# Kernel tuning notes

Measured on AMD Instinct MI355X. Metric: run time of the kernel, lower is better.

The kernel has to match this reference:

```python
import jax, jax.numpy as jnp
import numpy as np

D_MODEL = 1024
N_HEADS = 16
D_K = D_MODEL // N_HEADS
ROPE_BASE = 10000.0


def _rope_cos_sin(seq_len, dim):
    # matches calc_rope_theta: freqs over even indices of head dim
    freqs = jnp.arange(0, dim, 2, dtype=jnp.float32) / dim
    inv_freq = 1.0 / (ROPE_BASE ** freqs)                      # [dim/2]
    pos = jnp.arange(seq_len, dtype=jnp.float32)               # [S]
    ang = pos[:, None] * inv_freq[None, :]                     # [S, dim/2]
    return jnp.cos(ang), jnp.sin(ang)


def _apply_rope(x, cos, sin):
    # x: [N, S, dk]; complex pairs are consecutive elements (view_as_complex)
    x0 = x[..., 0::2]
    x1 = x[..., 1::2]
    r = x0 * cos - x1 * sin
    i = x0 * sin + x1 * cos
    return jnp.stack([r, i], axis=-1).reshape(x.shape)


def setup_inputs() -> dict:
    key = jax.random.key(0)
    ks = jax.random.split(key, 11)
    B, S, D = 4, 1024, D_MODEL
    w = lambda k: jax.random.normal(k, (D, D), dtype=jnp.float32) * 0.02
    b = lambda k: jax.random.normal(k, (D,), dtype=jnp.float32) * 0.02
    return {
        "q": jax.random.normal(ks[0], (B, S, D), dtype=jnp.float32),
        "k": jax.random.normal(ks[1], (B, S, D), dtype=jnp.float32),
        "v": jax.random.normal(ks[2], (B, S, D), dtype=jnp.float32),
        "Wq": w(ks[3]), "bq": b(ks[4]),
        "Wk": w(ks[5]), "bk": b(ks[6]),
        "Wv": w(ks[7]), "bv": b(ks[8]),
        "Wo": w(ks[9]), "bo": b(ks[10]),
    }


def reference(q, k, v, Wq, bq, Wk, bk, Wv, bv, Wo, bo):
    B, S, D = q.shape
    H, dk = N_HEADS, D_K
    qp = (q @ Wq + bq).reshape(B, S, H, dk)
    kp = (k @ Wk + bk).reshape(B, S, H, dk)
    vp = (v @ Wv + bv).reshape(B, S, H, dk)

    cos, sin = _rope_cos_sin(S, dk)
    # Faithful to source: raw reshape (B,S,H,dk)->(-1,S,dk) before RoPE
    qp = _apply_rope(qp.reshape(-1, S, dk), cos, sin).reshape(B, S, H, dk)
    kp = _apply_rope(kp.reshape(-1, S, dk), cos, sin).reshape(B, S, H, dk)

    qh = qp.transpose(0, 2, 1, 3)  # [B,H,S,dk]
    kh = kp.transpose(0, 2, 1, 3)
    vh = vp.transpose(0, 2, 1, 3)

    scores = jnp.einsum("bhqd,bhkd->bhqk", qh, kh) / jnp.sqrt(jnp.float32(dk))
    attn = jax.nn.softmax(scores, axis=-1)
    out = jnp.einsum("bhqk,bhkd->bhqd", attn, vh)
    out = out.transpose(0, 2, 1, 3).reshape(B, S, D)
    return out @ Wo + bo
```

## Files before the change

### kernel.cpp

```cpp
#include <hip/hip_runtime.h>

typedef __attribute__((ext_vector_type(8))) short bf16x8;
typedef __attribute__((ext_vector_type(4))) short short4v;
typedef __attribute__((ext_vector_type(4))) float f32x4;

#define MFMA16x16x32(a, b, c) __builtin_amdgcn_mfma_f32_16x16x32_bf16((a), (b), (c), 0, 0, 0)

__device__ __forceinline__ short f2bf(float f) {
    unsigned u = __builtin_bit_cast(unsigned, f);
    u += 0x7FFFu + ((u >> 16) & 1u);
    return (short)(u >> 16);
}

__device__ __forceinline__ void gl_lds16(const void* g, void* l) {
    __builtin_amdgcn_global_load_lds((__attribute__((address_space(1))) void*)g,
                                     (__attribute__((address_space(3))) void*)l,
                                     16, 0, 0);
}

__device__ __forceinline__ void cvt16(const float* __restrict__ p, bf16x8& lo, bf16x8& hi) {
    f32x4 a = *(const f32x4*)(p);
    f32x4 b = *(const f32x4*)(p + 4);
    f32x4 c = *(const f32x4*)(p + 8);
    f32x4 d = *(const f32x4*)(p + 12);
#pragma unroll
    for (int i = 0; i < 4; ++i) {
        lo[i]     = f2bf(a[i]);
        lo[i + 4] = f2bf(b[i]);
        hi[i]     = f2bf(c[i]);
        hi[i + 4] = f2bf(d[i]);
    }
}

__global__ __launch_bounds__(256) void cvt3(const float* __restrict__ x0,
                                            const float* __restrict__ x1,
                                            const float* __restrict__ x2,
                                            short* __restrict__ y) {
    int sel = blockIdx.y;
    const float* x = sel == 0 ? x0 : (sel == 1 ? x1 : x2);
    short* yy = y + (size_t)sel * (1 << 22);
    int i = (blockIdx.x * 256 + threadIdx.x) * 16;
    bf16x8 lo, hi;
    cvt16(x + i, lo, hi);
    *(bf16x8*)(yy + i)     = lo;
    *(bf16x8*)(yy + i + 8) = hi;
}

__global__ __launch_bounds__(256) void transW4(const float* __restrict__ w0,
                                               const float* __restrict__ w1,
                                               const float* __restrict__ w2,
                                               const float* __restrict__ w3,
                                               short* __restrict__ wt) {
    __shared__ short t[64][80];
    int z = blockIdx.z;
    const float* W = z == 0 ? w0 : (z == 1 ? w1 : (z == 2 ? w2 : w3));
    short* Wt = wt + (size_t)z * (1 << 20);
    int bx = blockIdx.x, by = blockIdx.y;
    int tid = threadIdx.x;
    int sr = tid >> 2, sc = (tid & 3) * 16;
    bf16x8 lo, hi;
    cvt16(W + (by * 64 + sr) * 1024 + bx * 64 + sc, lo, hi);
    *(bf16x8*)&t[sr][sc]     = lo;
    *(bf16x8*)&t[sr][sc + 8] = hi;
    __syncthreads();
    bf16x8 o0, o1;
#pragma unroll
    for (int i = 0; i < 8; ++i) {
        o0[i] = t[sc + i][sr];
        o1[i] = t[sc + 8 + i][sr];
    }
    short* dst = Wt + (bx * 64 + sr) * 1024 + by * 64 + sc;
    *(bf16x8*)(dst)     = o0;
    *(bf16x8*)(dst + 8) = o1;
}

template <int MODE>
__global__ __launch_bounds__(256) void gemm_nt(const short* __restrict__ A,
                                               const short* __restrict__ Bt,
                                               const float* __restrict__ bias,
                                               void* __restrict__ dstv) {
    __shared__ short As[128 * 64];
    __shared__ short Bs[64 * 64];
    const int K = 1024;
    int tid = threadIdx.x;
    int bn = blockIdx.x, bm = blockIdx.y;
    int wave = tid >> 6, lane = tid & 63;
    int quad = lane >> 4, l16 = lane & 15;
    int wm = (wave >> 1) * 64, wn = (wave & 1) * 32;

    f32x4 acc[4][2] = {};

    for (int kb = 0; kb < K; kb += 64) {
#pragma unroll
        for (int j = 0; j < 4; ++j) {
            int c = j * 256 + tid;
            gl_lds16(A + (bm * 128 + (c >> 3)) * K + kb + (c & 7) * 8, As + c * 8);
        }
#pragma unroll
        for (int j = 0; j < 2; ++j) {
            int c = j * 256 + tid;
            gl_lds16(Bt + (bn * 64 + (c >> 3)) * K + kb + (c & 7) * 8, Bs + c * 8);
        }
        __syncthreads();
#pragma unroll
        for (int ks = 0; ks < 2; ++ks) {
            bf16x8 bf0 = *(const bf16x8*)&Bs[(wn + l16) * 64 + ks * 32 + quad * 8];
            bf16x8 bf1 = *(const bf16x8*)&Bs[(wn + 16 + l16) * 64 + ks * 32 + quad * 8];
#pragma unroll
            for (int mi = 0; mi < 4; ++mi) {
                bf16x8 af = *(const bf16x8*)&As[(wm + mi * 16 + l16) * 64 + ks * 32 + quad * 8];
                acc[mi][0] = MFMA16x16x32(af, bf0, acc[mi][0]);
                acc[mi][1] = MFMA16x16x32(af, bf1, acc[mi][1]);
            }
        }
        __syncthreads();
    }

    int row0 = bm * 128 + wm;
    int col0 = bn * 64 + wn;
#pragma unroll
    for (int mi = 0; mi < 4; ++mi) {
#pragma unroll
        for (int ni = 0; ni < 2; ++ni) {
            int gn = col0 + ni * 16 + l16;
            float bv = bias[gn];
            f32x4 c = acc[mi][ni];
            if constexpr (MODE == 0) {
                short* dst = (short*)dstv;
                int h = gn >> 6, dd = gn & 63;
                float inv = exp2f(-(float)(dd >> 1) * 0.41524101186092029f);
#pragma unroll
                for (int r = 0; r < 4; ++r) {
                    int gm = row0 + mi * 16 + quad * 4 + r;
                    int s = gm & 1023, b = gm >> 10;
                    int p = ((s << 4) + h) & 1023;
                    float val = c[r] + bv;
                    float partner = __shfl_xor(val, 1);
                    float sn, cs;
                    __sincosf((float)p * inv, &sn, &cs);
                    float res = (dd & 1) ? fmaf(partner, sn, val * cs)
                                         : fmaf(val, cs, -(partner * sn));
                    dst[((b * 16 + h) * 1024 + s) * 64 + dd] = f2bf(res);
                }
            } else if constexpr (MODE == 2) {
                short* dst = (short*)dstv;
                int h = gn >> 6, dd = gn & 63;
                int gm0 = row0 + mi * 16 + quad * 4;
                int s0 = gm0 & 1023, b = gm0 >> 10;
                short4v pack;
#pragma unroll
                for (int r = 0; r < 4; ++r) pack[r] = f2bf(c[r] + bv);
                *(short4v*)&dst[((b * 16 + h) * 64 + dd) * 1024 + s0] = pack;
            } else {
                float* dst = (float*)dstv;
#pragma unroll
                for (int r = 0; r < 4; ++r) {
                    int gm = row0 + mi * 16 + quad * 4 + r;
                    dst[gm * 1024 + gn] = c[r] + bv;
                }
            }
        }
    }
}

__global__ __launch_bounds__(256) void attn_kernel(const short* __restrict__ Qh,
                                                   const short* __restrict__ Kh,
                                                   const short* __restrict__ Vt,
                                                   short* __restrict__ O) {
    __shared__ short Ks[2][32 * 64];
    __shared__ short Vs[2][64 * 32];
    __shared__ short Pl[4][32 * 32];
    int tid = threadIdx.x;
    int wave = tid >> 6, lane = tid & 63;
    int quad = lane >> 4, l16 = lane & 15;
    int bh = blockIdx.x >> 3, qt = blockIdx.x & 7;
    int qbase = qt * 128 + wave * 32;

    const short* Qp = Qh + (bh * 1024 + qbase) * 64;
    bf16x8 aq[2][2];
#pragma unroll
    for (int m = 0; m < 2; ++m)
#pragma unroll
        for (int kh = 0; kh < 2; ++kh)
            aq[m][kh] = *(const bf16x8*)&Qp[(m * 16 + l16) * 64 + kh * 32 + quad * 8];

    const short* Kp = Kh + bh * 1024 * 64;
    const short* Vp = Vt + bh * 64 * 1024;
    int ck = wave * 64 + lane;
    int vrow = ck >> 2, vcol = (ck & 3) * 8;

    float l_i[2][4] = {};
    f32x4 oa[2][4] = {};

    gl_lds16(Kp + ck * 8, &Ks[0][ck * 8]);
    gl_lds16(Vp + vrow * 1024 + vcol, &Vs[0][ck * 8]);
    __syncthreads();

    for (int kb = 0; kb < 1024; kb += 32) {
        int cur = (kb >> 5) & 1, nxt = cur ^ 1;
        int kb2 = (kb + 32) & 1023;
        gl_lds16(Kp + kb2 * 64 + ck * 8, &Ks[nxt][ck * 8]);
        gl_lds16(Vp + vrow * 1024 + kb2 + vcol, &Vs[nxt][ck * 8]);

        float pr[2][2][4];
#pragma unroll
        for (int g = 0; g < 2; ++g) {
            bf16x8 b0 = *(const bf16x8*)&Ks[cur][(g * 16 + l16) * 64 + quad * 8];
            bf16x8 b1 = *(const bf16x8*)&Ks[cur][(g * 16 + l16) * 64 + 32 + quad * 8];
#pragma unroll
            for (int m = 0; m < 2; ++m) {
                f32x4 s = {};
                s = MFMA16x16x32(aq[m][0], b0, s);
                s = MFMA16x16x32(aq[m][1], b1, s);
#pragma unroll
                for (int r = 0; r < 4; ++r) {
                    pr[m][g][r] = exp2f(s[r] * 0.18033688011112042f);
                    l_i[m][r] += pr[m][g][r];
                }
            }
        }
#pragma unroll
        for (int m = 0; m < 2; ++m)
#pragma unroll
            for (int g = 0; g < 2; ++g)
#pragma unroll
                for (int r = 0; r < 4; ++r)
                    Pl[wave][(m * 16 + quad * 4 + r) * 32 + g * 16 + l16] = f2bf(pr[m][g][r]);
        asm volatile("s_waitcnt lgkmcnt(0)" ::: "memory");
        bf16x8 ap0 = *(const bf16x8*)&Pl[wave][l16 * 32 + quad * 8];
        bf16x8 ap1 = *(const bf16x8*)&Pl[wave][(16 + l16) * 32 + quad * 8];
#pragma unroll
        for (int t = 0; t < 4; ++t) {
            bf16x8 bv = *(const bf16x8*)&Vs[cur][(t * 16 + l16) * 32 + quad * 8];
            oa[0][t] = MFMA16x16x32(ap0, bv, oa[0][t]);
            oa[1][t] = MFMA16x16x32(ap1, bv, oa[1][t]);
        }
        __syncthreads();
    }

#pragma unroll
    for (int d = 1; d < 16; d <<= 1)
#pragma unroll
        for (int m = 0; m < 2; ++m)
#pragma unroll
            for (int r = 0; r < 4; ++r) l_i[m][r] += __shfl_xor(l_i[m][r], d);

    int b = bh >> 4, h = bh & 15;
#pragma unroll
    for (int m = 0; m < 2; ++m)
#pragma unroll
        for (int t = 0; t < 4; ++t)
#pragma unroll
            for (int r = 0; r < 4; ++r) {
                int s = qbase + m * 16 + quad * 4 + r;
                O[(b * 1024 + s) * 1024 + h * 64 + t * 16 + l16] =
                    f2bf(oa[m][t][r] / l_i[m][r]);
            }
}

extern "C" void kernel_launch(void* const* d_in, const int* in_sizes, int n_in,
                              void* d_out, int out_size, void* d_ws, size_t ws_size,
                              hipStream_t stream) {
    const float* q  = (const float*)d_in[0];
    const float* k  = (const float*)d_in[1];
    const float* v  = (const float*)d_in[2];
    const float* Wq = (const float*)d_in[3];
    const float* bq = (const float*)d_in[4];
    const float* Wk = (const float*)d_in[5];
    const float* bk = (const float*)d_in[6];
    const float* Wv = (const float*)d_in[7];
    const float* bv = (const float*)d_in[8];
    const float* Wo = (const float*)d_in[9];
    const float* bo = (const float*)d_in[10];

    short* qb   = (short*)d_ws;
    short* kbuf = qb + (4 << 20);
    short* vb   = kbuf + (4 << 20);
    short* wt   = vb + (4 << 20);
    short* wtq  = wt;
    short* wtk  = wt + (1 << 20);
    short* wtv  = wt + (2 << 20);
    short* wto  = wt + (3 << 20);
    short* vt   = qb;
    short* obuf = kbuf;

    short* qh  = (short*)d_out;
    short* kh  = qh + (4 << 20);
    float* out = (float*)d_out;

    cvt3<<<dim3(1024, 3), 256, 0, stream>>>(q, k, v, qb);
    transW4<<<dim3(16, 16, 4), 256, 0, stream>>>(Wq, Wk, Wv, Wo, wt);

    dim3 ggrid(16, 32);
    gemm_nt<0><<<ggrid, 256, 0, stream>>>(qb,   wtq, bq, qh);
    gemm_nt<0><<<ggrid, 256, 0, stream>>>(kbuf, wtk, bk, kh);
    gemm_nt<2><<<ggrid, 256, 0, stream>>>(vb,   wtv, bv, vt);

    attn_kernel<<<512, 256, 0, stream>>>(qh, kh, vt, obuf);

    gemm_nt<3><<<ggrid, 256, 0, stream>>>(obuf, wto, bo, out);
}
```

Baseline: 249.1 us.

## Double-buffer GEMM LDS tiles and restructure attention with 8 waves and swizzled LDS

The GEMM kernel gets double-buffered LDS tiles, so the next K-slab loads are issued before computing on the current one. The attention kernel moves to 512 threads, with each wave owning 16 query rows, and K and V loads are split across thread halves. XOR-swizzled LDS layouts and a padded P buffer are meant to cut bank conflicts, and blocks are reordered so heads interleave across the grid. This trades per-wave register reuse for more waves, and doubles the GEMM LDS footprint, which may lower occupancy.

After: 242.1 us. 1.03x faster.

```diff
diff --git a/kernel.cpp b/kernel.cpp
--- a/kernel.cpp
+++ b/kernel.cpp
@@ -79,8 +79,8 @@
                                                const short* __restrict__ Bt,
                                                const float* __restrict__ bias,
                                                void* __restrict__ dstv) {
-    __shared__ short As[128 * 64];
-    __shared__ short Bs[64 * 64];
+    __shared__ short As[2][128 * 64];
+    __shared__ short Bs[2][64 * 64];
     const int K = 1024;
     int tid = threadIdx.x;
     int bn = blockIdx.x, bm = blockIdx.y;
@@ -90,25 +90,32 @@
 
     f32x4 acc[4][2] = {};
 
-    for (int kb = 0; kb < K; kb += 64) {
+    auto stage = [&](int b, int kb) {
 #pragma unroll
         for (int j = 0; j < 4; ++j) {
             int c = j * 256 + tid;
-            gl_lds16(A + (bm * 128 + (c >> 3)) * K + kb + (c & 7) * 8, As + c * 8);
+            gl_lds16(A + (bm * 128 + (c >> 3)) * K + kb + (c & 7) * 8, &As[b][c * 8]);
         }
 #pragma unroll
         for (int j = 0; j < 2; ++j) {
             int c = j * 256 + tid;
-            gl_lds16(Bt + (bn * 64 + (c >> 3)) * K + kb + (c & 7) * 8, Bs + c * 8);
-        }
-        __syncthreads();
+            gl_lds16(Bt + (bn * 64 + (c >> 3)) * K + kb + (c & 7) * 8, &Bs[b][c * 8]);
+        }
+    };
+
+    stage(0, 0);
+    __syncthreads();
+
+    for (int kb = 0; kb < K; kb += 64) {
+        int cur = (kb >> 6) & 1;
+        if (kb + 64 < K) stage(cur ^ 1, kb + 64);
 #pragma unroll
         for (int ks = 0; ks < 2; ++ks) {
-            bf16x8 bf0 = *(const bf16x8*)&Bs[(wn + l16) * 64 + ks * 32 + quad * 8];
-            bf16x8 bf1 = *(const bf16x8*)&Bs[(wn + 16 + l16) * 64 + ks * 32 + quad * 8];
+            bf16x8 bf0 = *(const bf16x8*)&Bs[cur][(wn + l16) * 64 + ks * 32 + quad * 8];
+            bf16x8 bf1 = *(const bf16x8*)&Bs[cur][(wn + 16 + l16) * 64 + ks * 32 + quad * 8];
 #pragma unroll
             for (int mi = 0; mi < 4; ++mi) {
-                bf16x8 af = *(const bf16x8*)&As[(wm + mi * 16 + l16) * 64 + ks * 32 + quad * 8];
+                bf16x8 af = *(const bf16x8*)&As[cur][(wm + mi * 16 + l16) * 64 + ks * 32 + quad * 8];
                 acc[mi][0] = MFMA16x16x32(af, bf0, acc[mi][0]);
                 acc[mi][1] = MFMA16x16x32(af, bf1, acc[mi][1]);
             }
@@ -163,99 +170,102 @@
     }
 }
 
-__global__ __launch_bounds__(256) void attn_kernel(const short* __restrict__ Qh,
+__global__ __launch_bounds__(512) void attn_kernel(const short* __restrict__ Qh,
                                                    const short* __restrict__ Kh,
                                                    const short* __restrict__ Vt,
                                                    short* __restrict__ O) {
     __shared__ short Ks[2][32 * 64];
     __shared__ short Vs[2][64 * 32];
-    __shared__ short Pl[4][32 * 32];
+    __shared__ short Pl[8][16 * 40];
     int tid = threadIdx.x;
     int wave = tid >> 6, lane = tid & 63;
     int quad = lane >> 4, l16 = lane & 15;
-    int bh = blockIdx.x >> 3, qt = blockIdx.x & 7;
-    int qbase = qt * 128 + wave * 32;
-
-    const short* Qp = Qh + (bh * 1024 + qbase) * 64;
-    bf16x8 aq[2][2];
-#pragma unroll
-    for (int m = 0; m < 2; ++m)
-#pragma unroll
-        for (int kh = 0; kh < 2; ++kh)
-            aq[m][kh] = *(const bf16x8*)&Qp[(m * 16 + l16) * 64 + kh * 32 + quad * 8];
+    int bh = blockIdx.x & 63, qt = blockIdx.x >> 6;
+    int qrow = qt * 128 + wave * 16;
+
+    const short* Qp = Qh + (bh * 1024 + qrow) * 64;
+    bf16x8 aq[2];
+#pragma unroll
+    for (int kh = 0; kh < 2; ++kh)
+        aq[kh] = *(const bf16x8*)&Qp[l16 * 64 + kh * 32 + quad * 8];
 
     const short* Kp = Kh + bh * 1024 * 64;
     const short* Vp = Vt + bh * 64 * 1024;
-    int ck = wave * 64 + lane;
-    int vrow = ck >> 2, vcol = (ck & 3) * 8;
-
-    float l_i[2][4] = {};
-    f32x4 oa[2][4] = {};
-
-    gl_lds16(Kp + ck * 8, &Ks[0][ck * 8]);
-    gl_lds16(Vp + vrow * 1024 + vcol, &Vs[0][ck * 8]);
+
+    int ck = tid & 255;
+    bool isV = tid >= 256;
+    int krow = ck >> 3;
+    int vrow = ck >> 2;
+    int ksrc = krow * 64 + (((ck & 7) ^ (krow & 7)) * 8);
+    int vsrc = vrow * 1024 + ((((ck & 3) ^ (vrow & 3) ^ ((vrow >> 2) & 3)) & 3) * 8);
+
+    int ksw  = l16 & 7;
+    int vswr = (l16 & 3) ^ ((l16 >> 2) & 3);
+
+    float l_i[4] = {};
+    f32x4 oa[4] = {};
+
+    if (!isV) gl_lds16(Kp + ksrc, &Ks[0][ck * 8]);
+    else      gl_lds16(Vp + vsrc, &Vs[0][ck * 8]);
     __syncthreads();
+
+    short* Pw = &Pl[wave][0];
 
     for (int kb = 0; kb < 1024; kb += 32) {
         int cur = (kb >> 5) & 1, nxt = cur ^ 1;
         int kb2 = (kb + 32) & 1023;
-        gl_lds16(Kp + kb2 * 64 + ck * 8, &Ks[nxt][ck * 8]);
-        gl_lds16(Vp + vrow * 1024 + kb2 + vcol, &Vs[nxt][ck * 8]);
-
-        float pr[2][2][4];
+        if (!isV) gl_lds16(Kp + kb2 * 64 + ksrc, &Ks[nxt][ck * 8]);
+        else      gl_lds16(Vp + kb2 + vsrc,      &Vs[nxt][ck * 8]);
+
 #pragma unroll
         for (int g = 0; g < 2; ++g) {
-            bf16x8 b0 = *(const bf16x8*)&Ks[cur][(g * 16 + l16) * 64 + quad * 8];
-            bf16x8 b1 = *(const bf16x8*)&Ks[cur][(g * 16 + l16) * 64 + 32 + quad * 8];
-#pragma unroll
-            for (int m = 0; m < 2; ++m) {
-                f32x4 s = {};
-                s = MFMA16x16x32(aq[m][0], b0, s);
-                s = MFMA16x16x32(aq[m][1], b1, s);
-#pragma unroll
-                for (int r = 0; r < 4; ++r) {
-                    pr[m][g][r] = exp2f(s[r] * 0.18033688011112042f);
-                    l_i[m][r] += pr[m][g][r];
-                }
+            f32x4 s = {};
+#pragma unroll
+            for (int kh = 0; kh < 2; ++kh) {
+                bf16x8 bk = *(const bf16x8*)
+                    &Ks[cur][(g * 16 + l16) * 64 + (((kh * 4 + quad) ^ ksw) * 8)];
+                s = MFMA16x16x32(aq[kh], bk, s);
             }
-        }
-#pragma unroll
-        for (int m = 0; m < 2; ++m)
-#pragma unroll
-            for (int g = 0; g < 2; ++g)
-#pragma unroll
-                for (int r = 0; r < 4; ++r)
-                    Pl[wave][(m * 16 + quad * 4 + r) * 32 + g * 16 + l16] = f2bf(pr[m][g][r]);
+#pragma unroll
+            for (int r = 0; r < 4; ++r) {
+                float p = exp2f(s[r] * 0.18033688011112042f);
+                l_i[r] += p;
+                Pw[(quad * 4 + r) * 40 + g * 16 + l16] = f2bf(p);
+            }
+        }
+
+        bf16x8 bv[4];
+#pragma unroll
+        for (int t = 0; t < 4; ++t)
+            bv[t] = *(const bf16x8*)&Vs[cur][(t * 16 + l16) * 32 + ((quad ^ vswr) * 8)];
+
         asm volatile("s_waitcnt lgkmcnt(0)" ::: "memory");
-        bf16x8 ap0 = *(const bf16x8*)&Pl[wave][l16 * 32 + quad * 8];
-        bf16x8 ap1 = *(const bf16x8*)&Pl[wave][(16 + l16) * 32 + quad * 8];
-#pragma unroll
-        for (int t = 0; t < 4; ++t) {
-            bf16x8 bv = *(const bf16x8*)&Vs[cur][(t * 16 + l16) * 32 + quad * 8];
-            oa[0][t] = MFMA16x16x32(ap0, bv, oa[0][t]);
-            oa[1][t] = MFMA16x16x32(ap1, bv, oa[1][t]);
-        }
+        bf16x8 ap = *(const bf16x8*)&Pw[l16 * 40 + quad * 8];
+
+#pragma unroll
+        for (int t = 0; t < 4; ++t)
+            oa[t] = MFMA16x16x32(ap, bv[t], oa[t]);
+
         __syncthreads();
     }
 
 #pragma unroll
     for (int d = 1; d < 16; d <<= 1)
 #pragma unroll
-        for (int m = 0; m < 2; ++m)
-#pragma unroll
-            for (int r = 0; r < 4; ++r) l_i[m][r] += __shfl_xor(l_i[m][r], d);
+        for (int r = 0; r < 4; ++r) l_i[r] += __shfl_xor(l_i[r], d);
+
+    float inv[4];
+#pragma unroll
+    for (int r = 0; r < 4; ++r) inv[r] = 1.0f / l_i[r];
 
     int b = bh >> 4, h = bh & 15;
 #pragma unroll
-    for (int m = 0; m < 2; ++m)
-#pragma unroll
-        for (int t = 0; t < 4; ++t)
-#pragma unroll
-            for (int r = 0; r < 4; ++r) {
-                int s = qbase + m * 16 + quad * 4 + r;
-                O[(b * 1024 + s) * 1024 + h * 64 + t * 16 + l16] =
-                    f2bf(oa[m][t][r] / l_i[m][r]);
-            }
+    for (int t = 0; t < 4; ++t)
+#pragma unroll
+        for (int r = 0; r < 4; ++r) {
+            int s = qrow + quad * 4 + r;
+            O[(b * 1024 + s) * 1024 + h * 64 + t * 16 + l16] = f2bf(oa[t][r] * inv[r]);
+        }
 }
 
 extern "C" void kernel_launch(void* const* d_in, const int* in_sizes, int n_in,
@@ -296,7 +306,7 @@
     gemm_nt<0><<<ggrid, 256, 0, stream>>>(kbuf, wtk, bk, kh);
     gemm_nt<2><<<ggrid, 256, 0, stream>>>(vb,   wtv, bv, vt);
 
-    attn_kernel<<<512, 256, 0, stream>>>(qh, kh, vt, obuf);
+    attn_kernel<<<512, 512, 0, stream>>>(qh, kh, vt, obuf);
 
     gemm_nt<3><<<ggrid, 256, 0, stream>>>(obuf, wto, bo, out);
 }
```
